# Kernel tuning notes

Hardware: AMD Instinct MI355X
Metric: run time of the kernel (lower is better)

The kernel has to match this reference:

```python
import jax, jax.numpy as jnp
import numpy as np

B = 524288
D_IN = 128
H = 16          # hard-coded by amax slicing in MLSTMCell
D_OUT = 4


def _quant(x, amax):
    # torch quant_tensor: clamp(round(x * 127/amax), -127, 127) -> int8 (kept as
    # integer-valued float32 here; exact since |v| <= 127)
    if amax.ndim > 1:
        amax = jnp.squeeze(amax, 1)
    return jnp.clip(jnp.round(x * (127.0 / amax)), -127.0, 127.0)


def _dequant(x, amax, double=False):
    max_range = 127.0 ** 2 if double else 127.0
    scale = max_range / amax
    if scale.ndim > 1:
        scale = jnp.squeeze(scale, 1)
    return x / scale


def setup_inputs() -> dict:
    key = jax.random.key(0)
    ks = jax.random.split(key, 13)
    # weights are stored pre-quantized int8 (integer-valued); torch casts them
    # to int32 before matmul, so integer-valued float32 is bit-exact in fp32
    intw = lambda k, shp: jax.random.randint(k, shp, -127, 128).astype(jnp.float32)
    x = jax.random.normal(ks[0], (B, D_IN), dtype=jnp.float32)
    h = jax.random.normal(ks[1], (B, H), dtype=jnp.float32) * 0.1
    c = jax.random.normal(ks[2], (B, H), dtype=jnp.float32) * 0.1
    w1 = intw(ks[3], (H, D_IN))          # net.0.weight
    w_ih = intw(ks[4], (4 * H, H))       # lstm.weight_ih
    w_hh = intw(ks[5], (4 * H, H))       # lstm.weight_hh
    w_out = intw(ks[6], (D_OUT, H))      # output_layer.weight
    u = lambda k, shp, lo, hi: jax.random.uniform(k, shp, minval=lo, maxval=hi, dtype=jnp.float32)
    amax_in0 = u(ks[7], (), 1.0, 4.0)            # net.0._input_quantizer._amax (per-tensor)
    amax_w0 = u(ks[8], (H, 1), 32.0, 127.0)      # net.0._weight_quantizer._amax (per-channel)
    amax_lstm_in = u(ks[9], (), 1.0, 4.0)        # lstm._input_quantizer._amax
    amax_w_lstm = u(ks[10], (4 * H, 1), 32.0, 127.0)  # lstm._weight_quantizer._amax
    amax_out_in = u(ks[11], (), 1.0, 4.0)        # output_layer._input_quantizer._amax
    amax_w_out = u(ks[12], (D_OUT, 1), 32.0, 127.0)   # output_layer._weight_quantizer._amax
    return dict(x=x, h=h, c=c, w1=w1, w_ih=w_ih, w_hh=w_hh, w_out=w_out,
                amax_in0=amax_in0, amax_w0=amax_w0, amax_lstm_in=amax_lstm_in,
                amax_w_lstm=amax_w_lstm, amax_out_in=amax_out_in, amax_w_out=amax_w_out)


def reference(x, h, c, w1, w_ih, w_hh, w_out, amax_in0, amax_w0,
              amax_lstm_in, amax_w_lstm, amax_out_in, amax_w_out):
    # --- fc_1: quantize input, int matmul, relu, requantize for lstm ---
    xq = _quant(x, amax_in0)                     # [B, D_IN] int8-valued
    a = xq @ w1.T                                # [B, H] int32-valued (exact in fp32)
    a = jnp.maximum(a, 0.0)                      # relu
    a = _quant(_dequant(a, amax_in0 * amax_w0, double=True), amax_lstm_in)  # [B, H]
    # --- quantize hidden state (hc arrives as float) ---
    hq = _quant(h, amax_lstm_in)
    cq = _quant(c, amax_lstm_in)
    # --- MLSTMCell ---
    amax = amax_lstm_in * amax_w_lstm            # [4H, 1]
    gates = a @ w_ih.T + hq @ w_hh.T             # [B, 4H] int32-valued
    gates = _dequant(gates, amax, double=True)
    i, f, g, o = jnp.split(gates, 4, axis=1)
    gates = jnp.concatenate([jax.nn.sigmoid(i), jax.nn.sigmoid(f),
                             jnp.tanh(g), jax.nn.sigmoid(o)], axis=1)
    gq = _quant(gates, amax)                     # [B, 4H] int8-valued
    i, f, g, o = jnp.split(gq, 4, axis=1)
    cy = (_dequant(f * cq, amax[16:32] * 3.4764, double=True)
          + _dequant(i * g, amax[:16] * amax[32:48], double=True))
    od = _dequant(o, amax[48:], double=False)
    hy = od * jnp.tanh(cy)
    # --- output layer ---
    xo = _quant(hy, amax_out_in) @ w_out.T       # [B, D_OUT]
    xo = _dequant(xo, amax_out_in * amax_w_out, double=True)
    return xo, hy, cy
```

## Files before the change

### kernel.cpp

```cpp
#include <hip/hip_runtime.h>
#include <math.h>
#include <limits.h>


#define OFF_QS    0
#define OFF_SFC1  4
#define OFF_SG    20
#define OFF_QG    84
#define OFF_SCF   148
#define OFF_SCIG  164
#define OFF_SOD   180
#define OFF_SXO   196
#define OFF_VBG   200
#define OFF_TI    216
#define OFF_TF    280
#define OFF_TO    344
#define OFF_TG    408
#define OFF_IGT   536
#define OFF_ODT   1064
#define OFF_W1P   1192
#define OFF_WIHP  1704
#define OFF_WHHP  1960
#define OFF_WOUTP 2216

__device__ __forceinline__ float qclip(float v) {
    return fminf(fmaxf(v, -127.0f), 127.0f);
}

__device__ __forceinline__ int sdot4(int a, int b, int c) {
#if __has_builtin(__builtin_amdgcn_sdot4)
    return __builtin_amdgcn_sdot4(a, b, c, false);
#else
    c += ((a << 24) >> 24) * ((b << 24) >> 24);
    c += ((a << 16) >> 24) * ((b << 16) >> 24);
    c += ((a << 8)  >> 24) * ((b << 8)  >> 24);
    c += (a >> 24) * (b >> 24);
    return c;
#endif
}

__device__ __forceinline__ int pack4i(int a, int b, int c, int d) {
    return (a & 255) | ((b & 255) << 8) | ((c & 255) << 16) | (d << 24);
}

__device__ __forceinline__ int pack4f(const float* p) {
    return pack4i((int)p[0], (int)p[1], (int)p[2], (int)p[3]);
}

typedef __attribute__((address_space(1))) const void g_void;
typedef __attribute__((address_space(3))) void l_void;

__device__ __forceinline__ void stage16(const float* g, float* l) {
    __builtin_amdgcn_global_load_lds((g_void*)g, (l_void*)l, 16, 0, 0);
}

#define WAIT_VM0()   { asm volatile("s_waitcnt vmcnt(0)" ::: "memory"); __builtin_amdgcn_sched_barrier(0); }
#define WAIT_LGKM0() { asm volatile("s_waitcnt lgkmcnt(0)" ::: "memory"); __builtin_amdgcn_sched_barrier(0); }

__device__ __forceinline__ int qeval_sig(int gi, float s, float q) {
    float v = (float)gi / s;
    float a = 1.0f / (1.0f + expf(-v));
    return (int)qclip(rintf(a * q));
}
__device__ __forceinline__ int qeval_tanh(int gi, float s, float q) {
    float v = (float)gi / s;
    float a = tanhf(v);
    return (int)qclip(rintf(a * q));
}

#define GLIM 1048576

__device__ int search_thr_sig(float s, float q, int target) {
    if (qeval_sig(GLIM, s, q) < target) return INT_MAX;
    int lo = -GLIM, hi = GLIM;
    while (hi - lo > 1) {
        int mid = lo + ((hi - lo) >> 1);
        if (qeval_sig(mid, s, q) >= target) hi = mid; else lo = mid;
    }
    return hi;
}
__device__ int search_thr_tanh(float s, float q, int target) {
    if (qeval_tanh(GLIM, s, q) < target) return INT_MAX;
    int lo = -GLIM, hi = GLIM;
    while (hi - lo > 1) {
        int mid = lo + ((hi - lo) >> 1);
        if (qeval_tanh(mid, s, q) >= target) hi = mid; else lo = mid;
    }
    return hi;
}

__global__ void __launch_bounds__(1024) setup_all(
    const float* __restrict__ w1, const float* __restrict__ w_ih,
    const float* __restrict__ w_hh, const float* __restrict__ w_out,
    const float* __restrict__ a_in0, const float* __restrict__ a_w0,
    const float* __restrict__ a_lstm, const float* __restrict__ a_wl,
    const float* __restrict__ a_out, const float* __restrict__ a_wo,
    float* __restrict__ wsf)
{
    const int t = threadIdx.x;
    int* wsi = (int*)wsf;
    const float amax_in0 = a_in0[0], amax_lstm = a_lstm[0], amax_out = a_out[0];

    if (t == 0) {
        wsf[OFF_QS + 0] = 127.0f / amax_in0;
        wsf[OFF_QS + 1] = 127.0f / amax_lstm;
        wsf[OFF_QS + 2] = 127.0f / amax_out;
    }
    if (t < 16) wsf[OFF_SFC1 + t] = 16129.0f / (amax_in0 * a_w0[t]);
    if (t < 64) {
        float am = amax_lstm * a_wl[t];
        wsf[OFF_SG + t] = 16129.0f / am;
        wsf[OFF_QG + t] = 127.0f / am;
    }
    if (t < 16) {
        float amf = amax_lstm * a_wl[16 + t];
        wsf[OFF_SCF + t] = 16129.0f / (amf * 3.4764f);
        float amo = amax_lstm * a_wl[48 + t];
        wsf[OFF_SOD + t] = 127.0f / amo;
        float ami = amax_lstm * a_wl[t];
        float amg = amax_lstm * a_wl[32 + t];
        wsf[OFF_SCIG + t] = 16129.0f / (ami * amg);
        float s = 16129.0f / amg, q = 127.0f / amg;
        wsi[OFF_VBG + t] = qeval_tanh(-GLIM, s, q);
    }
    if (t < 4) wsf[OFF_SXO + t] = 16129.0f / (amax_out * a_wo[t]);

    if (t < 512) {
        int kc = t >> 6, q = (t >> 4) & 3, j = t & 15;
        wsi[OFF_W1P + t] = pack4f(w1 + j * 128 + kc * 16 + q * 4);
    }
    if (t < 256) { wsi[OFF_WIHP + t] = pack4f(w_ih + 4 * t);
                   wsi[OFF_WHHP + t] = pack4f(w_hh + 4 * t); }
    if (t < 16)  wsi[OFF_WOUTP + t] = pack4f(w_out + 4 * t);

    if (t < 64) {
        int m = t >> 2, k = t & 3;
        float am = amax_lstm * a_wl[m];
        wsi[OFF_TI + t] = search_thr_sig(16129.0f / am, 127.0f / am, k + 1);
    } else if (t < 128) {
        int u = t - 64, m = u >> 2, k = u & 3;
        float am = amax_lstm * a_wl[16 + m];
        wsi[OFF_TF + u] = search_thr_sig(16129.0f / am, 127.0f / am, k + 1);
    } else if (t < 192) {
        int u = t - 128, m = u >> 2, k = u & 3;
        float am = amax_lstm * a_wl[48 + m];
        wsi[OFF_TO + u] = search_thr_sig(16129.0f / am, 127.0f / am, k + 1);
    } else if (t < 320) {
        int u = t - 192, m = u >> 3, k = u & 7;
        float am = amax_lstm * a_wl[32 + m];
        float s = 16129.0f / am, q = 127.0f / am;
        int vb = qeval_tanh(-GLIM, s, q);
        wsi[OFF_TG + u] = search_thr_tanh(s, q, vb + 1 + k);
    } else if (t < 848) {
        int u = t - 320, m = u / 33, p = u % 33;
        float ami = amax_lstm * a_wl[m];
        float amg = amax_lstm * a_wl[32 + m];
        float scig = 16129.0f / (ami * amg);
        wsf[OFF_IGT + u] = (float)(p - 16) / scig;
    } else if (t < 928) {
        int u = t - 848, m = u / 5, oq = u % 5;
        float amo = amax_lstm * a_wl[48 + m];
        float sod = 127.0f / amo;
        wsf[OFF_ODT + m * 8 + oq] = (float)oq / sod;
    }
}

__global__ void __launch_bounds__(256, 8) mlpq_kernel(
    const float* __restrict__ x, const float* __restrict__ h, const float* __restrict__ c,
    const float* __restrict__ wsf,
    float* __restrict__ out_xo, float* __restrict__ out_hy, float* __restrict__ out_cy,
    int nrows)
{
    __shared__ float s_tab[656];
    __shared__ __align__(1024) float s_stage[4][1024];

    for (int i = threadIdx.x; i < 656; i += 256) s_tab[i] = wsf[OFF_IGT + i];
    __syncthreads();
    const float* s_igt = s_tab;
    const float* s_odt = s_tab + 528;

    const int tid = threadIdx.x;
    const int wv  = tid >> 6;
    const int rl  = tid & 63;
    const int wrow0 = blockIdx.x * 256 + wv * 64;
    const int r = wrow0 + rl;

    const int sw = (rl >> 1) & 3;
    const int qs_stage = (rl & 3) ^ ((rl >> 3) & 3);
    const int rstage = wrow0 + (rl >> 2);

    float* buf = &s_stage[wv][0];
    const float4* buf4 = reinterpret_cast<const float4*>(buf);

    const int* __restrict__ wsi = (const int*)wsf;
    const float qs_in   = wsf[OFF_QS + 0];
    const float qs_lstm = wsf[OFF_QS + 1];
    const float qs_out  = wsf[OFF_QS + 2];

    const float* gph = h + (size_t)rstage * 16 + qs_stage * 4;
    const float* gpc = c + (size_t)rstage * 16 + qs_stage * 4;
    const float* gpx = x + (size_t)rstage * 128 + qs_stage * 4;

    stage16(gph + 0 * 256, buf + 0 * 256);
    stage16(gph + 1 * 256, buf + 1 * 256);
    stage16(gph + 2 * 256, buf + 2 * 256);
    stage16(gph + 3 * 256, buf + 3 * 256);
    WAIT_VM0();
    float4 hv[4];
#pragma unroll
    for (int q = 0; q < 4; ++q) hv[q] = buf4[rl * 4 + (q ^ sw)];
    WAIT_LGKM0();
    stage16(gpx + 0 * 2048, buf + 0 * 256);
    stage16(gpx + 1 * 2048, buf + 1 * 256);
    stage16(gpx + 2 * 2048, buf + 2 * 256);
    stage16(gpx + 3 * 2048, buf + 3 * 256);
    int hql[4];
#pragma unroll
    for (int q = 0; q < 4; ++q) {
        float4 v = hv[q];
        hql[q] = pack4i((int)qclip(rintf(v.x * qs_lstm)),
                        (int)qclip(rintf(v.y * qs_lstm)),
                        (int)qclip(rintf(v.z * qs_lstm)),
                        (int)qclip(rintf(v.w * qs_lstm)));
    }

    int acc[16];
#pragma unroll
    for (int j = 0; j < 16; ++j) acc[j] = 0;

#pragma unroll 1
    for (int kc = 0; kc < 7; ++kc) {
        WAIT_VM0();
        float4 xv[4];
#pragma unroll
        for (int q = 0; q < 4; ++q) xv[q] = buf4[rl * 4 + (q ^ sw)];
        WAIT_LGKM0();
        const float* g = gpx + (kc + 1) * 16;
        stage16(g + 0 * 2048, buf + 0 * 256);
        stage16(g + 1 * 2048, buf + 1 * 256);
        stage16(g + 2 * 2048, buf + 2 * 256);
        stage16(g + 3 * 2048, buf + 3 * 256);
#pragma unroll
        for (int q = 0; q < 4; ++q) {
            float4 v = xv[q];
            int w = pack4i((int)qclip(rintf(v.x * qs_in)),
                           (int)qclip(rintf(v.y * qs_in)),
                           (int)qclip(rintf(v.z * qs_in)),
                           (int)qclip(rintf(v.w * qs_in)));
            const int* wrow = wsi + OFF_W1P + kc * 64 + q * 16;
#pragma unroll
            for (int j = 0; j < 16; ++j)
                acc[j] = sdot4(w, wrow[j], acc[j]);
        }
    }
    {
        WAIT_VM0();
        float4 xv[4];
#pragma unroll
        for (int q = 0; q < 4; ++q) xv[q] = buf4[rl * 4 + (q ^ sw)];
        WAIT_LGKM0();
        stage16(gpc + 0 * 256, buf + 0 * 256);
        stage16(gpc + 1 * 256, buf + 1 * 256);
        stage16(gpc + 2 * 256, buf + 2 * 256);
        stage16(gpc + 3 * 256, buf + 3 * 256);
#pragma unroll
        for (int q = 0; q < 4; ++q) {
            float4 v = xv[q];
            int w = pack4i((int)qclip(rintf(v.x * qs_in)),
                           (int)qclip(rintf(v.y * qs_in)),
                           (int)qclip(rintf(v.z * qs_in)),
                           (int)qclip(rintf(v.w * qs_in)));
            const int* wrow = wsi + OFF_W1P + 7 * 64 + q * 16;
#pragma unroll
            for (int j = 0; j < 16; ++j)
                acc[j] = sdot4(w, wrow[j], acc[j]);
        }
    }

    int aql[4];
#pragma unroll
    for (int jg = 0; jg < 4; ++jg) {
        int q[4];
#pragma unroll
        for (int u = 0; u < 4; ++u) {
            int j = jg * 4 + u;
            int ai = acc[j] > 0 ? acc[j] : 0;
            float dq = (float)ai / wsf[OFF_SFC1 + j];
            q[u] = (int)qclip(rintf(dq * qs_lstm));
        }
        aql[jg] = pack4i(q[0], q[1], q[2], q[3]);
    }

    WAIT_VM0();

    float4* __restrict__ hyrow = reinterpret_cast<float4*>(out_hy) + (size_t)r * 4;
    float4* __restrict__ cyrow = reinterpret_cast<float4*>(out_cy) + (size_t)r * 4;
    int xql[4];

#pragma unroll
    for (int mg = 0; mg < 4; ++mg) {
        float4 cv = buf4[rl * 4 + (mg ^ sw)];
        float cvals[4] = {cv.x, cv.y, cv.z, cv.w};
        float hy4[4], cy4[4];
        int xq4[4];
#pragma unroll
        for (int t = 0; t < 4; ++t) {
            const int m = mg * 4 + t;
            int gi = 0, gf = 0, gg = 0, go = 0;
#pragma unroll
            for (int p = 0; p < 4; ++p) {
                int ap = aql[p], hp = hql[p];
                gi = sdot4(ap, wsi[OFF_WIHP + (m)      * 4 + p], gi);
                gi = sdot4(hp, wsi[OFF_WHHP + (m)      * 4 + p], gi);
                gf = sdot4(ap, wsi[OFF_WIHP + (m + 16) * 4 + p], gf);
                gf = sdot4(hp, wsi[OFF_WHHP + (m + 16) * 4 + p], gf);
                gg = sdot4(ap, wsi[OFF_WIHP + (m + 32) * 4 + p], gg);
                gg = sdot4(hp, wsi[OFF_WHHP + (m + 32) * 4 + p], gg);
                go = sdot4(ap, wsi[OFF_WIHP + (m + 48) * 4 + p], go);
                go = sdot4(hp, wsi[OFF_WHHP + (m + 48) * 4 + p], go);
            }
            int iq = (gi >= wsi[OFF_TI + m * 4 + 0]) + (gi >= wsi[OFF_TI + m * 4 + 1])
                   + (gi >= wsi[OFF_TI + m * 4 + 2]) + (gi >= wsi[OFF_TI + m * 4 + 3]);
            int fq = (gf >= wsi[OFF_TF + m * 4 + 0]) + (gf >= wsi[OFF_TF + m * 4 + 1])
                   + (gf >= wsi[OFF_TF + m * 4 + 2]) + (gf >= wsi[OFF_TF + m * 4 + 3]);
            int oq = (go >= wsi[OFF_TO + m * 4 + 0]) + (go >= wsi[OFF_TO + m * 4 + 1])
                   + (go >= wsi[OFF_TO + m * 4 + 2]) + (go >= wsi[OFF_TO + m * 4 + 3]);
            int gq = wsi[OFF_VBG + m]
                   + (gg >= wsi[OFF_TG + m * 8 + 0]) + (gg >= wsi[OFF_TG + m * 8 + 1])
                   + (gg >= wsi[OFF_TG + m * 8 + 2]) + (gg >= wsi[OFF_TG + m * 8 + 3])
                   + (gg >= wsi[OFF_TG + m * 8 + 4]) + (gg >= wsi[OFF_TG + m * 8 + 5])
                   + (gg >= wsi[OFF_TG + m * 8 + 6]) + (gg >= wsi[OFF_TG + m * 8 + 7]);

            int cqv = (int)qclip(rintf(cvals[t] * qs_lstm));

            float cy = (float)(fq * cqv) / wsf[OFF_SCF + m]
                     + s_igt[m * 33 + (iq * gq + 16)];
            float od = s_odt[m * 8 + oq];
            float hy = od * tanhf(cy);

            hy4[t] = hy;
            cy4[t] = cy;
            xq4[t] = (int)qclip(rintf(hy * qs_out));
        }
        hyrow[mg] = make_float4(hy4[0], hy4[1], hy4[2], hy4[3]);
        cyrow[mg] = make_float4(cy4[0], cy4[1], cy4[2], cy4[3]);
        xql[mg] = pack4i(xq4[0], xq4[1], xq4[2], xq4[3]);
    }

    float4 xov;
    {
        int s0 = 0, s1 = 0, s2 = 0, s3 = 0;
#pragma unroll
        for (int p = 0; p < 4; ++p) {
            s0 = sdot4(xql[p], wsi[OFF_WOUTP + 0 * 4 + p], s0);
            s1 = sdot4(xql[p], wsi[OFF_WOUTP + 1 * 4 + p], s1);
            s2 = sdot4(xql[p], wsi[OFF_WOUTP + 2 * 4 + p], s2);
            s3 = sdot4(xql[p], wsi[OFF_WOUTP + 3 * 4 + p], s3);
        }
        xov.x = (float)s0 / wsf[OFF_SXO + 0];
        xov.y = (float)s1 / wsf[OFF_SXO + 1];
        xov.z = (float)s2 / wsf[OFF_SXO + 2];
        xov.w = (float)s3 / wsf[OFF_SXO + 3];
    }
    reinterpret_cast<float4*>(out_xo)[r] = xov;
}

extern "C" void kernel_launch(void* const* d_in, const int* in_sizes, int n_in,
                              void* d_out, int out_size, void* d_ws, size_t ws_size,
                              hipStream_t stream) {
    const float* x      = (const float*)d_in[0];
    const float* h      = (const float*)d_in[1];
    const float* c      = (const float*)d_in[2];
    const float* w1     = (const float*)d_in[3];
    const float* w_ih   = (const float*)d_in[4];
    const float* w_hh   = (const float*)d_in[5];
    const float* w_out  = (const float*)d_in[6];
    const float* a_in0  = (const float*)d_in[7];
    const float* a_w0   = (const float*)d_in[8];
    const float* a_lstm = (const float*)d_in[9];
    const float* a_wl   = (const float*)d_in[10];
    const float* a_out  = (const float*)d_in[11];
    const float* a_wo   = (const float*)d_in[12];

    const int B = in_sizes[0] / 128;
    float* out    = (float*)d_out;
    float* out_xo = out;
    float* out_hy = out + (size_t)B * 4;
    float* out_cy = out + (size_t)B * 20;
    float* wsf    = (float*)d_ws;

    hipLaunchKernelGGL(setup_all, dim3(1), dim3(1024), 0, stream,
                       w1, w_ih, w_hh, w_out, a_in0, a_w0, a_lstm, a_wl, a_out, a_wo, wsf);

    dim3 block(256);
    dim3 grid((B + 255) / 256);
    hipLaunchKernelGGL(mlpq_kernel, grid, block, 0, stream,
                       x, h, c, wsf, out_xo, out_hy, out_cy, B);
}
```

Before: 124.0 us.

## Load x via registers, quantize cooperatively, stage int8 rows in LDS

The kernel no longer streams x, h and c through global_load_lds staging with 7 serialized waits. Each group of four lanes now issues coalesced float4 register loads for 16 rows at a time, quantizes them to packed int8, and writes them into a swizzled LDS buffer. Each thread then reads back its own 32 packed words and does the first layer as a straight 32-step sdot4 chain, with the weight packing reordered to row-major to match. h and c are loaded directly per row, and launch bounds drop to 4 waves per SIMD to make room for the extra registers, which may lower occupancy and latency hiding.

```diff
diff --git a/kernel.cpp b/kernel.cpp
--- a/kernel.cpp
+++ b/kernel.cpp
@@ -47,14 +47,11 @@
     return pack4i((int)p[0], (int)p[1], (int)p[2], (int)p[3]);
 }
 
-typedef __attribute__((address_space(1))) const void g_void;
-typedef __attribute__((address_space(3))) void l_void;
-
-__device__ __forceinline__ void stage16(const float* g, float* l) {
-    __builtin_amdgcn_global_load_lds((g_void*)g, (l_void*)l, 16, 0, 0);
-}
-
-#define WAIT_VM0()   { asm volatile("s_waitcnt vmcnt(0)" ::: "memory"); __builtin_amdgcn_sched_barrier(0); }
+__device__ __forceinline__ int quantpack(float4 v, float qs) {
+    return pack4i((int)qclip(rintf(v.x * qs)), (int)qclip(rintf(v.y * qs)),
+                  (int)qclip(rintf(v.z * qs)), (int)qclip(rintf(v.w * qs)));
+}
+
 #define WAIT_LGKM0() { asm volatile("s_waitcnt lgkmcnt(0)" ::: "memory"); __builtin_amdgcn_sched_barrier(0); }
 
 __device__ __forceinline__ int qeval_sig(int gi, float s, float q) {
@@ -125,10 +122,7 @@
     }
     if (t < 4) wsf[OFF_SXO + t] = 16129.0f / (amax_out * a_wo[t]);
 
-    if (t < 512) {
-        int kc = t >> 6, q = (t >> 4) & 3, j = t & 15;
-        wsi[OFF_W1P + t] = pack4f(w1 + j * 128 + kc * 16 + q * 4);
-    }
+    if (t < 512) wsi[OFF_W1P + t] = pack4f(w1 + 4 * t);
     if (t < 256) { wsi[OFF_WIHP + t] = pack4f(w_ih + 4 * t);
                    wsi[OFF_WHHP + t] = pack4f(w_hh + 4 * t); }
     if (t < 16)  wsi[OFF_WOUTP + t] = pack4f(w_out + 4 * t);
@@ -165,14 +159,14 @@
     }
 }
 
-__global__ void __launch_bounds__(256, 8) mlpq_kernel(
+__global__ void __launch_bounds__(256, 4) mlpq_kernel(
     const float* __restrict__ x, const float* __restrict__ h, const float* __restrict__ c,
     const float* __restrict__ wsf,
     float* __restrict__ out_xo, float* __restrict__ out_hy, float* __restrict__ out_cy,
     int nrows)
 {
     __shared__ float s_tab[656];
-    __shared__ __align__(1024) float s_stage[4][1024];
+    __shared__ __align__(16) int s_xq[4][2048];
 
     for (int i = threadIdx.x; i < 656; i += 256) s_tab[i] = wsf[OFF_IGT + i];
     __syncthreads();
@@ -185,113 +179,102 @@
     const int wrow0 = blockIdx.x * 256 + wv * 64;
     const int r = wrow0 + rl;
 
-    const int sw = (rl >> 1) & 3;
-    const int qs_stage = (rl & 3) ^ ((rl >> 3) & 3);
-    const int rstage = wrow0 + (rl >> 2);
-
-    float* buf = &s_stage[wv][0];
-    const float4* buf4 = reinterpret_cast<const float4*>(buf);
+    const int qd = rl & 3;
+    const int g  = rl >> 2;
+
+    int* bufi = &s_xq[wv][0];
 
     const int* __restrict__ wsi = (const int*)wsf;
     const float qs_in   = wsf[OFF_QS + 0];
     const float qs_lstm = wsf[OFF_QS + 1];
     const float qs_out  = wsf[OFF_QS + 2];
 
-    const float* gph = h + (size_t)rstage * 16 + qs_stage * 4;
-    const float* gpc = c + (size_t)rstage * 16 + qs_stage * 4;
-    const float* gpx = x + (size_t)rstage * 128 + qs_stage * 4;
-
-    stage16(gph + 0 * 256, buf + 0 * 256);
-    stage16(gph + 1 * 256, buf + 1 * 256);
-    stage16(gph + 2 * 256, buf + 2 * 256);
-    stage16(gph + 3 * 256, buf + 3 * 256);
-    WAIT_VM0();
-    float4 hv[4];
-#pragma unroll
-    for (int q = 0; q < 4; ++q) hv[q] = buf4[rl * 4 + (q ^ sw)];
+    const float4* __restrict__ xb = reinterpret_cast<const float4*>(x);
+
+    float4 xr0[8], xr1[8];
+    {
+        const size_t ro = (size_t)(wrow0 + 0 * 16 + g) * 32 + qd;
+#pragma unroll
+        for (int s = 0; s < 8; ++s) xr0[s] = xb[ro + s * 4];
+    }
+    {
+        const size_t ro = (size_t)(wrow0 + 1 * 16 + g) * 32 + qd;
+#pragma unroll
+        for (int s = 0; s < 8; ++s) xr1[s] = xb[ro + s * 4];
+    }
+
+#define PROC_SUBITER(I, REG, RELOAD)                                         \
+    {                                                                        \
+        const int rp  = (I) * 16 + g;                                        \
+        const int wb  = rp * 32;                                             \
+        const int swz = (rp & 7) << 2;                                       \
+        int pw[8];                                                           \
+        _Pragma("unroll")                                                    \
+        for (int s = 0; s < 8; ++s) pw[s] = quantpack(REG[s], qs_in);        \
+        _Pragma("unroll")                                                    \
+        for (int s = 0; s < 8; ++s)                                          \
+            bufi[wb + ((s * 4 + qd) ^ swz)] = pw[s];                         \
+        if (RELOAD) {                                                        \
+            const size_t ro2 = (size_t)(wrow0 + ((I) + 2) * 16 + g) * 32 + qd;\
+            _Pragma("unroll")                                                \
+            for (int s = 0; s < 8; ++s) REG[s] = xb[ro2 + s * 4];            \
+        }                                                                    \
+    }
+
+    PROC_SUBITER(0, xr0, 1)
+    PROC_SUBITER(1, xr1, 1)
+    PROC_SUBITER(2, xr0, 0)
+    PROC_SUBITER(3, xr1, 0)
+#undef PROC_SUBITER
+
+    float4 hv4[4], cv4[4];
+    {
+        const float4* hb = reinterpret_cast<const float4*>(h) + (size_t)r * 4;
+        const float4* cb = reinterpret_cast<const float4*>(c) + (size_t)r * 4;
+#pragma unroll
+        for (int jg = 0; jg < 4; ++jg) { hv4[jg] = hb[jg]; cv4[jg] = cb[jg]; }
+    }
+
     WAIT_LGKM0();
-    stage16(gpx + 0 * 2048, buf + 0 * 256);
-    stage16(gpx + 1 * 2048, buf + 1 * 256);
-    stage16(gpx + 2 * 2048, buf + 2 * 256);
-    stage16(gpx + 3 * 2048, buf + 3 * 256);
-    int hql[4];
-#pragma unroll
-    for (int q = 0; q < 4; ++q) {
-        float4 v = hv[q];
-        hql[q] = pack4i((int)qclip(rintf(v.x * qs_lstm)),
-                        (int)qclip(rintf(v.y * qs_lstm)),
-                        (int)qclip(rintf(v.z * qs_lstm)),
-                        (int)qclip(rintf(v.w * qs_lstm)));
+
+    int xw[32];
+    {
+        const int4* b4 = reinterpret_cast<const int4*>(bufi);
+#pragma unroll
+        for (int t = 0; t < 8; ++t) {
+            int4 vv = b4[rl * 8 + (t ^ (rl & 7))];
+            xw[t * 4 + 0] = vv.x; xw[t * 4 + 1] = vv.y;
+            xw[t * 4 + 2] = vv.z; xw[t * 4 + 3] = vv.w;
+        }
     }
 
     int acc[16];
 #pragma unroll
-    for (int j = 0; j < 16; ++j) acc[j] = 0;
-
-#pragma unroll 1
-    for (int kc = 0; kc < 7; ++kc) {
-        WAIT_VM0();
-        float4 xv[4];
-#pragma unroll
-        for (int q = 0; q < 4; ++q) xv[q] = buf4[rl * 4 + (q ^ sw)];
-        WAIT_LGKM0();
-        const float* g = gpx + (kc + 1) * 16;
-        stage16(g + 0 * 2048, buf + 0 * 256);
-        stage16(g + 1 * 2048, buf + 1 * 256);
-        stage16(g + 2 * 2048, buf + 2 * 256);
-        stage16(g + 3 * 2048, buf + 3 * 256);
-#pragma unroll
-        for (int q = 0; q < 4; ++q) {
-            float4 v = xv[q];
-            int w = pack4i((int)qclip(rintf(v.x * qs_in)),
-                           (int)qclip(rintf(v.y * qs_in)),
-                           (int)qclip(rintf(v.z * qs_in)),
-                           (int)qclip(rintf(v.w * qs_in)));
-            const int* wrow = wsi + OFF_W1P + kc * 64 + q * 16;
-#pragma unroll
-            for (int j = 0; j < 16; ++j)
-                acc[j] = sdot4(w, wrow[j], acc[j]);
-        }
-    }
-    {
-        WAIT_VM0();
-        float4 xv[4];
-#pragma unroll
-        for (int q = 0; q < 4; ++q) xv[q] = buf4[rl * 4 + (q ^ sw)];
-        WAIT_LGKM0();
-        stage16(gpc + 0 * 256, buf + 0 * 256);
-        stage16(gpc + 1 * 256, buf + 1 * 256);
-        stage16(gpc + 2 * 256, buf + 2 * 256);
-        stage16(gpc + 3 * 256, buf + 3 * 256);
-#pragma unroll
-        for (int q = 0; q < 4; ++q) {
-            float4 v = xv[q];
-            int w = pack4i((int)qclip(rintf(v.x * qs_in)),
-                           (int)qclip(rintf(v.y * qs_in)),
-                           (int)qclip(rintf(v.z * qs_in)),
-                           (int)qclip(rintf(v.w * qs_in)));
-            const int* wrow = wsi + OFF_W1P + 7 * 64 + q * 16;
-#pragma unroll
-            for (int j = 0; j < 16; ++j)
-                acc[j] = sdot4(w, wrow[j], acc[j]);
-        }
+    for (int j = 0; j < 16; ++j) {
+        int a = 0;
+        const int* wrow = wsi + OFF_W1P + j * 32;
+#pragma unroll
+        for (int k = 0; k < 32; ++k) a = sdot4(xw[k], wrow[k], a);
+        acc[j] = a;
     }
 
     int aql[4];
 #pragma unroll
     for (int jg = 0; jg < 4; ++jg) {
-        int q[4];
+        int qv[4];
 #pragma unroll
         for (int u = 0; u < 4; ++u) {
             int j = jg * 4 + u;
             int ai = acc[j] > 0 ? acc[j] : 0;
             float dq = (float)ai / wsf[OFF_SFC1 + j];
-            q[u] = (int)qclip(rintf(dq * qs_lstm));
+            qv[u] = (int)qclip(rintf(dq * qs_lstm));
         }
-        aql[jg] = pack4i(q[0], q[1], q[2], q[3]);
-    }
-
-    WAIT_VM0();
+        aql[jg] = pack4i(qv[0], qv[1], qv[2], qv[3]);
+    }
+
+    int hql[4];
+#pragma unroll
+    for (int jg = 0; jg < 4; ++jg) hql[jg] = quantpack(hv4[jg], qs_lstm);
 
     float4* __restrict__ hyrow = reinterpret_cast<float4*>(out_hy) + (size_t)r * 4;
     float4* __restrict__ cyrow = reinterpret_cast<float4*>(out_cy) + (size_t)r * 4;
@@ -299,7 +282,7 @@
 
 #pragma unroll
     for (int mg = 0; mg < 4; ++mg) {
-        float4 cv = buf4[rl * 4 + (mg ^ sw)];
+        float4 cv = cv4[mg];
         float cvals[4] = {cv.x, cv.y, cv.z, cv.w};
         float hy4[4], cy4[4];
         int xq4[4];
```

Result: faster. 120.2 us (-3.1%).
